# Kernel tuning notes

Hardware: AMD Instinct MI355X
Metric: run time of the kernel (lower is better)

Reference implementation:

```python
import jax, jax.numpy as jnp
import numpy as np

NUM = 5          # spline intervals
KS = 3           # spline order k
GRID_LO, GRID_HI = -1.0, 1.0
KH = KW = 3      # kernel size
STRIDE = 1
PAD = 1
DIL = 1


def make_grid():
    # extended uniform grid: num+2k+1 points from lo-k*h to hi+k*h (h=(hi-lo)/num)
    h = (GRID_HI - GRID_LO) / NUM
    return GRID_LO + jnp.arange(-KS, NUM + KS + 1, dtype=jnp.float32) * h  # (12,)


def b_spline_basis(x, grid, k):
    # x: (..., ), grid: (G,) shared across features (all rows of pykan grid identical)
    # returns (..., G-1-k) Cox-de Boor bases of order k
    x = x[..., None]
    B = ((x >= grid[:-1]) & (x < grid[1:])).astype(x.dtype)
    for p in range(1, k + 1):
        left = (x - grid[:-(p + 1)]) / (grid[p:-1] - grid[:-(p + 1)]) * B[..., :-1]
        right = (grid[p + 1:] - x) / (grid[p + 1:] - grid[1:-p]) * B[..., 1:]
        B = left + right
    return B


def extract_patches(x):
    # torch.nn.Unfold ordering: (B, C, kh*kw, OH, OW), kernel positions row-major
    x = jnp.pad(x, ((0, 0), (0, 0), (PAD, PAD), (PAD, PAD)))
    B, C, H, W = x.shape
    OH = (H - DIL * (KH - 1) - 1) // STRIDE + 1
    OW = (W - DIL * (KW - 1) - 1) // STRIDE + 1
    pats = []
    for i in range(KH):
        for j in range(KW):
            pats.append(x[:, :, i * DIL:i * DIL + STRIDE * (OH - 1) + 1:STRIDE,
                          j * DIL:j * DIL + STRIDE * (OW - 1) + 1:STRIDE])
    return jnp.stack(pats, axis=2)  # (B, C, K, OH, OW)


def setup_inputs() -> dict:
    key = jax.random.key(0)
    k1, k2, k3, k4, k5 = jax.random.split(key, 5)
    B, C, O, H, W = 8, 32, 64, 32, 32
    K, M = KH * KW, NUM + KS
    x = jax.random.normal(k1, (B, C, H, W), dtype=jnp.float32)
    coef = jax.random.normal(k2, (O, C, K, M), dtype=jnp.float32) * 0.1
    scale_base = jax.random.normal(k3, (O, C, K), dtype=jnp.float32) / np.sqrt(K)
    scale_sp = jnp.ones((O, C, K), dtype=jnp.float32)
    bias = jnp.zeros((O,), dtype=jnp.float32)
    return {"x": x, "coef": coef, "scale_base": scale_base,
            "scale_sp": scale_sp, "bias": bias}


def reference(x, coef, scale_base, scale_sp, bias):
    grid = make_grid()
    p = extract_patches(x)                              # (B, C, K, OH, OW)
    B, C, K, OH, OW = p.shape
    t = p.transpose(0, 1, 3, 4, 2).reshape(B, C, OH * OW, K)  # (B, C, L, K)
    Bsp = b_spline_basis(t, grid, KS)                   # (B, C, L, K, M)
    silu = t * jax.nn.sigmoid(t)
    W_sp = scale_sp[..., None] * coef                   # (O, C, K, M)
    out = (jnp.einsum('bclk,ock->bol', silu, scale_base)
           + jnp.einsum('bclkm,ockm->bol', Bsp, W_sp))
    out = out + bias[None, :, None]
    return out.reshape(B, -1, OH, OW)
```

## Files before the change

### kernel.cpp

```cpp
#include <hip/hip_runtime.h>


typedef __attribute__((ext_vector_type(8))) short v8s;
typedef __attribute__((ext_vector_type(4))) float v4f;
typedef unsigned short ushort_t;

#define WB_ELEMS    (64u * 2592u)
#define CELL_STRIDE 296
#define ROW_STRIDE  (34 * CELL_STRIDE)

__device__ __forceinline__ unsigned short f2bf(float v) {
  union { float f; unsigned int u; } w; w.f = v;
  unsigned int r = w.u + 0x7FFFu + ((w.u >> 16) & 1u);
  return (unsigned short)(r >> 16);
}

__global__ __launch_bounds__(256) void kan_prep(const float* __restrict__ coef,
                                                const float* __restrict__ sb,
                                                const float* __restrict__ ssp,
                                                ushort_t* __restrict__ Wb) {
  int i = blockIdx.x * 256 + threadIdx.x;
  if (i >= (int)WB_ELEMS) return;
  int o = i / 2592;
  int r = i - o * 2592;
  int pos = r / 288;
  int rj = r - pos * 288;
  int j = rj >> 5;
  int c = rj & 31;
  int sidx = (o * 32 + c) * 9 + pos;
  float val = (j == 0) ? sb[sidx] : ssp[sidx] * coef[sidx * 8 + (j - 1)];
  Wb[i] = f2bf(val);
}

template <int LO, int HI>
__device__ __forceinline__ void kloop(const ushort_t* __restrict__ fb,
                                      const ushort_t* __restrict__ wp,
                                      v4f& acc0, v4f& acc1) {
#pragma unroll
  for (int s = LO; s < HI; ++s) {
    const int di = s / 27;
    const int dj = (s / 9) % 3;
    const int kk = s % 9;
    const int fo = di * ROW_STRIDE + dj * CELL_STRIDE + kk * 32;
    v8s wf = *(const v8s*)(wp + s * 32);
    v8s a0 = *(const v8s*)(fb + fo);
    v8s a1 = *(const v8s*)(fb + fo + 16 * CELL_STRIDE);
    acc0 = __builtin_amdgcn_mfma_f32_16x16x32_bf16(wf, a0, acc0, 0, 0, 0);
    acc1 = __builtin_amdgcn_mfma_f32_16x16x32_bf16(wf, a1, acc1, 0, 0, 0);
  }
}

__global__ __launch_bounds__(512, 4) void kan_fused(const float* __restrict__ x,
                                                    const ushort_t* __restrict__ Wb,
                                                    const float* __restrict__ bias,
                                                    float* __restrict__ out) {
  __shared__ ushort_t feat[3 * ROW_STRIDE];
  __shared__ float xs[32 * 33];

  const int tid = threadIdx.x;
  const int bx = blockIdx.x;
  const int ohalf = bx & 1;
  const int oh = (bx >> 1) & 31;
  const int b = bx >> 6;

  for (int r = 0; r < 3; ++r) {
    const int h = oh + r - 1;
    const bool hval = (h >= 0) && (h < 32);
    if (hval) {
      int idx = tid * 2;
      int c = idx >> 5, w = idx & 31;
      float2 v = *(const float2*)(x + (((b * 32 + c) * 32 + h) * 32 + w));
      xs[c * 33 + w] = v.x;
      xs[c * 33 + w + 1] = v.y;
    }
    __syncthreads();
    for (int idx = tid; idx < 1088; idx += 512) {
      int c = idx & 31, cell = idx >> 5;
      int wi = cell - 1;
      float t = 0.0f;
      if (hval && wi >= 0 && wi < 32) t = xs[c * 33 + wi];

      unsigned short f0 = f2bf(t / (1.0f + __expf(-t)));
      float u  = (t + 2.2f) * 2.5f;
      float fi = floorf(u);
      int   i  = (int)fi;
      float s  = u - fi;
      float s2 = s * s, s3 = s2 * s;
      float om = 1.0f - s;
      float w0 = om * om * om * (1.0f / 6.0f);
      float w1 = (4.0f - 6.0f * s2 + 3.0f * s3) * (1.0f / 6.0f);
      float w2 = (1.0f + 3.0f * s + 3.0f * s2 - 3.0f * s3) * (1.0f / 6.0f);
      float w3 = s3 * (1.0f / 6.0f);

      ushort_t* dst = feat + r * ROW_STRIDE + cell * CELL_STRIDE + c;
      dst[0] = f0;
#pragma unroll
      for (int jj = 0; jj < 8; ++jj) {
        int d = jj - i + 3;
        float bv = (d == 0) ? w0 : (d == 1) ? w1 : (d == 2) ? w2 : (d == 3) ? w3 : 0.0f;
        dst[(jj + 1) * 32] = f2bf(bv);
      }
    }
    __syncthreads();
  }

  const int wv   = tid >> 6;
  const int lane = tid & 63;
  const int row  = lane & 15;
  const int quad = lane >> 4;
  const int og   = wv & 1;
  const int kq   = wv >> 1;
  const int obase = ohalf * 32 + og * 16;

  const ushort_t* fb = feat + row * CELL_STRIDE + quad * 8;
  const ushort_t* wp = Wb + (size_t)(obase + row) * 2592 + quad * 8;

  v4f acc0 = {0.f, 0.f, 0.f, 0.f};
  v4f acc1 = acc0;

  if (kq == 0)      kloop<0, 20>(fb, wp, acc0, acc1);
  else if (kq == 1) kloop<20, 40>(fb, wp, acc0, acc1);
  else if (kq == 2) kloop<40, 60>(fb, wp, acc0, acc1);
  else              kloop<60, 81>(fb, wp, acc0, acc1);

  __syncthreads();
  float* red = (float*)feat;
  if (kq != 0) {
    float* rp = red + ((kq - 1) * 2 + og) * 512 + quad * 4 * 32 + row;
#pragma unroll
    for (int r = 0; r < 4; ++r) {
      rp[r * 32]      = acc0[r];
      rp[r * 32 + 16] = acc1[r];
    }
  }
  __syncthreads();
  if (kq == 0) {
    float* o0 = out + ((size_t)(b * 64 + obase + quad * 4)) * 1024 + oh * 32 + row;
#pragma unroll
    for (int r = 0; r < 4; ++r) {
      float bv = bias[obase + quad * 4 + r];
      float s0 = acc0[r], s1 = acc1[r];
#pragma unroll
      for (int gs = 0; gs < 3; ++gs) {
        const float* rp = red + (gs * 2 + og) * 512 + (quad * 4 + r) * 32 + row;
        s0 += rp[0];
        s1 += rp[16];
      }
      o0[(size_t)r * 1024]      = s0 + bv;
      o0[(size_t)r * 1024 + 16] = s1 + bv;
    }
  }
}

extern "C" void kernel_launch(void* const* d_in, const int* in_sizes, int n_in,
                              void* d_out, int out_size, void* d_ws, size_t ws_size,
                              hipStream_t stream) {
  const float* x    = (const float*)d_in[0];
  const float* coef = (const float*)d_in[1];
  const float* sb   = (const float*)d_in[2];
  const float* ssp  = (const float*)d_in[3];
  const float* bias = (const float*)d_in[4];
  float* out = (float*)d_out;

  ushort_t* Wb = (ushort_t*)d_ws;

  hipLaunchKernelGGL(kan_prep, dim3(648), dim3(256), 0, stream, coef, sb, ssp, Wb);
  hipLaunchKernelGGL(kan_fused, dim3(512), dim3(512), 0, stream, x, Wb, bias, out);
}
```

Before: 82.47 us.

## Cover all 64 outputs per block and stage weight prep through shared memory

The fused kernel now runs 1024-thread blocks that each compute all 64 output channels for one output row, not half of them. This halves the grid and stops the B-spline feature tile from being built twice per row. The feature tile is zeroed up front, so each input writes only its 4 nonzero basis values, with out-of-range ones sent to a dump buffer. The prep kernel now uses one block per output channel, reads coef coalesced, transposes through LDS and writes 32-bit words. Risks: 256 blocks may underfill the GPU's CUs, and the larger blocks strain register limits.

```diff
diff --git a/kernel.cpp b/kernel.cpp
--- a/kernel.cpp
+++ b/kernel.cpp
@@ -3,9 +3,9 @@
 
 typedef __attribute__((ext_vector_type(8))) short v8s;
 typedef __attribute__((ext_vector_type(4))) float v4f;
+typedef __attribute__((ext_vector_type(4))) int   v4i;
 typedef unsigned short ushort_t;
 
-#define WB_ELEMS    (64u * 2592u)
 #define CELL_STRIDE 296
 #define ROW_STRIDE  (34 * CELL_STRIDE)
 
@@ -19,17 +19,31 @@
                                                 const float* __restrict__ sb,
                                                 const float* __restrict__ ssp,
                                                 ushort_t* __restrict__ Wb) {
-  int i = blockIdx.x * 256 + threadIdx.x;
-  if (i >= (int)WB_ELEMS) return;
-  int o = i / 2592;
-  int r = i - o * 2592;
-  int pos = r / 288;
-  int rj = r - pos * 288;
-  int j = rj >> 5;
-  int c = rj & 31;
-  int sidx = (o * 32 + c) * 9 + pos;
-  float val = (j == 0) ? sb[sidx] : ssp[sidx] * coef[sidx * 8 + (j - 1)];
-  Wb[i] = f2bf(val);
+  __shared__ ushort_t row_[2592];
+  const int o   = blockIdx.x;
+  const int tid = threadIdx.x;
+  const float* cf   = coef + o * 2304;
+  const float* sspo = ssp  + o * 288;
+  const float* sbo  = sb   + o * 288;
+
+#pragma unroll
+  for (int k = 0; k < 9; ++k) {
+    int l   = k * 256 + tid;
+    int c   = l / 72;
+    int rem = l - c * 72;
+    int pos = rem >> 3;
+    int m   = rem & 7;
+    float v = sspo[c * 9 + pos] * cf[l];
+    row_[(pos * 9 + m + 1) * 32 + c] = f2bf(v);
+  }
+  for (int t = tid; t < 288; t += 256) {
+    int c = t / 9, pos = t - c * 9;
+    row_[(pos * 9) * 32 + c] = f2bf(sbo[t]);
+  }
+  __syncthreads();
+  unsigned int* dst = (unsigned int*)(Wb + (size_t)o * 2592);
+  const unsigned int* src = (const unsigned int*)row_;
+  for (int i = tid; i < 1296; i += 256) dst[i] = src[i];
 }
 
 template <int LO, int HI>
@@ -50,31 +64,38 @@
   }
 }
 
-__global__ __launch_bounds__(512, 4) void kan_fused(const float* __restrict__ x,
-                                                    const ushort_t* __restrict__ Wb,
-                                                    const float* __restrict__ bias,
-                                                    float* __restrict__ out) {
-  __shared__ ushort_t feat[3 * ROW_STRIDE];
+__global__ __launch_bounds__(1024, 4) void kan_fused(const float* __restrict__ x,
+                                                     const ushort_t* __restrict__ Wb,
+                                                     const float* __restrict__ bias,
+                                                     float* __restrict__ out) {
+  __shared__ __align__(16) ushort_t feat[3 * ROW_STRIDE];
   __shared__ float xs[32 * 33];
+  __shared__ ushort_t dump[64];
 
   const int tid = threadIdx.x;
-  const int bx = blockIdx.x;
-  const int ohalf = bx & 1;
-  const int oh = (bx >> 1) & 31;
-  const int b = bx >> 6;
+  const int bx  = blockIdx.x;
+  const int oh  = bx & 31;
+  const int b   = bx >> 5;
+
+  {
+    v4i z = {0, 0, 0, 0};
+    v4i* fz = (v4i*)feat;
+#pragma unroll
+    for (int k = 0; k < 4; ++k) {
+      int i = tid + k * 1024;
+      if (i < 3774) fz[i] = z;
+    }
+  }
 
   for (int r = 0; r < 3; ++r) {
     const int h = oh + r - 1;
     const bool hval = (h >= 0) && (h < 32);
     if (hval) {
-      int idx = tid * 2;
-      int c = idx >> 5, w = idx & 31;
-      float2 v = *(const float2*)(x + (((b * 32 + c) * 32 + h) * 32 + w));
-      xs[c * 33 + w] = v.x;
-      xs[c * 33 + w + 1] = v.y;
+      int c = tid >> 5, w = tid & 31;
+      xs[c * 33 + w] = x[(((b * 32 + c) * 32 + h) * 32 + w)];
     }
     __syncthreads();
-    for (int idx = tid; idx < 1088; idx += 512) {
+    for (int idx = tid; idx < 1088; idx += 1024) {
       int c = idx & 31, cell = idx >> 5;
       int wi = cell - 1;
       float t = 0.0f;
@@ -92,13 +113,15 @@
       float w2 = (1.0f + 3.0f * s + 3.0f * s2 - 3.0f * s3) * (1.0f / 6.0f);
       float w3 = s3 * (1.0f / 6.0f);
 
-      ushort_t* dst = feat + r * ROW_STRIDE + cell * CELL_STRIDE + c;
-      dst[0] = f0;
+      ushort_t* cb = feat + r * ROW_STRIDE + cell * CELL_STRIDE + c;
+      cb[0] = f0;
 #pragma unroll
-      for (int jj = 0; jj < 8; ++jj) {
-        int d = jj - i + 3;
-        float bv = (d == 0) ? w0 : (d == 1) ? w1 : (d == 2) ? w2 : (d == 3) ? w3 : 0.0f;
-        dst[(jj + 1) * 32] = f2bf(bv);
+      for (int d = 0; d < 4; ++d) {
+        float wv_ = (d == 0) ? w0 : (d == 1) ? w1 : (d == 2) ? w2 : w3;
+        int jj = i - 3 + d;
+        ushort_t* p = ((unsigned)jj <= 7u) ? (cb + (jj + 1) * 32)
+                                           : (dump + (tid & 63));
+        *p = f2bf(wv_);
       }
     }
     __syncthreads();
@@ -108,9 +131,9 @@
   const int lane = tid & 63;
   const int row  = lane & 15;
   const int quad = lane >> 4;
-  const int og   = wv & 1;
-  const int kq   = wv >> 1;
-  const int obase = ohalf * 32 + og * 16;
+  const int og   = wv & 3;
+  const int kq   = wv >> 2;
+  const int obase = og * 16;
 
   const ushort_t* fb = feat + row * CELL_STRIDE + quad * 8;
   const ushort_t* wp = Wb + (size_t)(obase + row) * 2592 + quad * 8;
@@ -126,7 +149,7 @@
   __syncthreads();
   float* red = (float*)feat;
   if (kq != 0) {
-    float* rp = red + ((kq - 1) * 2 + og) * 512 + quad * 4 * 32 + row;
+    float* rp = red + ((kq - 1) * 4 + og) * 512 + quad * 4 * 32 + row;
 #pragma unroll
     for (int r = 0; r < 4; ++r) {
       rp[r * 32]      = acc0[r];
@@ -142,7 +165,7 @@
       float s0 = acc0[r], s1 = acc1[r];
 #pragma unroll
       for (int gs = 0; gs < 3; ++gs) {
-        const float* rp = red + (gs * 2 + og) * 512 + (quad * 4 + r) * 32 + row;
+        const float* rp = red + (gs * 4 + og) * 512 + (quad * 4 + r) * 32 + row;
         s0 += rp[0];
         s1 += rp[16];
       }
@@ -164,6 +187,6 @@
 
   ushort_t* Wb = (ushort_t*)d_ws;
 
-  hipLaunchKernelGGL(kan_prep, dim3(648), dim3(256), 0, stream, coef, sb, ssp, Wb);
-  hipLaunchKernelGGL(kan_fused, dim3(512), dim3(512), 0, stream, x, Wb, bias, out);
+  hipLaunchKernelGGL(kan_prep, dim3(64), dim3(256), 0, stream, coef, sb, ssp, Wb);
+  hipLaunchKernelGGL(kan_fused, dim3(256), dim3(1024), 0, stream, x, Wb, bias, out);
 }
```

After: 75.22 us. 8.8% less time.
